# Performance work log

Measured on AMD Instinct MI355X. Metric: run time of the kernel, lower is better.

The kernel has to match this reference:

```python
import jax, jax.numpy as jnp
import numpy as np

VOCAB = 64
EMB = 128
H = 256
OUT = 1
NUM_IN = 7
NUM_OUT = 4
B = 64
S = 2048
D_IN = EMB + NUM_OUT  # input_dim to the 1x1 convs


def setup_inputs() -> dict:
    key = jax.random.key(0)
    ks = jax.random.split(key, 12)
    ev = jax.random.randint(ks[0], (B, S, 1), 0, VOCAB).astype(jnp.float32)
    num = jax.random.normal(ks[1], (B, S, NUM_IN), dtype=jnp.float32)
    X = jnp.concatenate([ev, num], axis=-1)  # [B,S,1+NUM_IN]
    sc = lambda fan_in: 1.0 / np.sqrt(fan_in)
    return {
        "X": X,
        "emb": jax.random.normal(ks[2], (VOCAB, EMB), dtype=jnp.float32),
        "num_W": jax.random.normal(ks[3], (NUM_IN, NUM_OUT), dtype=jnp.float32) * sc(NUM_IN),
        "num_b": jnp.zeros((NUM_OUT,), jnp.float32),
        "Wf": jax.random.normal(ks[4], (D_IN, 3 * H), dtype=jnp.float32) * sc(D_IN),
        "bf": jnp.zeros((3 * H,), jnp.float32),
        "Wb": jax.random.normal(ks[5], (D_IN, 3 * H), dtype=jnp.float32) * sc(D_IN),
        "bb": jnp.zeros((3 * H,), jnp.float32),
        "Mu": jax.random.normal(ks[6], (2 * H, 1), dtype=jnp.float32) * sc(2 * H),
        "out_W": jax.random.normal(ks[7], (2 * H, OUT), dtype=jnp.float32) * sc(2 * H),
        "out_b": jnp.zeros((OUT,), jnp.float32),
    }


def _fo_pool(conv_out):
    # conv_out: [B, S, 3H] (already time-ordered as desired). Returns [B, S, H]
    Z, F, O = jnp.split(conv_out, 3, axis=-1)  # O computed but unused (as in source)
    Z = jnp.tanh(Z)
    F = jax.nn.sigmoid(F)
    # scan over time with state [B, H]
    Zt = jnp.swapaxes(Z, 0, 1)  # [S,B,H]
    Ft = jnp.swapaxes(F, 0, 1)
    h0 = jnp.zeros(Z.shape[::2][:1] + Z.shape[2:], Z.dtype) if False else jnp.zeros((Z.shape[0], Z.shape[2]), Z.dtype)
    def step(h, zf):
        z, f = zf
        h = f * h + (1.0 - f) * z
        return h, h
    _, hs = jax.lax.scan(step, h0, (Zt, Ft))  # [S,B,H] in scan order
    return jnp.swapaxes(hs, 0, 1)  # [B,S,H]


def reference(X, emb, num_W, num_b, Wf, bf, Wb, bb, Mu, out_W, out_b):
    ev = X[:, :, 0].astype(jnp.int32)            # event ids
    num = X[:, :, 1:]                             # numeric features [B,S,7]
    e = emb[ev]                                   # [B,S,EMB]
    n = num @ num_W + num_b                       # [B,S,NUM_OUT]
    x = jnp.concatenate([e, n], axis=-1)          # [B,S,D_IN]
    cf = x @ Wf + bf                              # 1x1 conv == pointwise linear, [B,S,3H]
    cb = x @ Wb + bb
    h_fwd = _fo_pool(cf)                          # [B,S,H], time order
    # backward direction: source iterates t = S-1..0 and stacks in append order
    h_bwd = _fo_pool(cb[:, ::-1, :])              # [B,S,H], reversed-time order (faithful)
    hc = jnp.concatenate([h_fwd, h_bwd], axis=-1) # [B,S,2H]
    scores = hc @ Mu                              # [B,S,1]
    w = jax.nn.softmax(scores, axis=1)
    ctx = jnp.sum(hc * w, axis=1)                 # [B,2H]
    return ctx @ out_W + out_b                    # [B,OUT]
```

## Files before the change

kernel.cpp:

```cpp
#include <hip/hip_runtime.h>
#include <stdint.h>

#define VOCABN 64
#define EMBN   128
#define HDIM   256
#define NUMIN  7
#define BN     64
#define SN     2048
#define TWOH   512
#define SEG    32
#define SEGLEN 64

#define CZ 2.8853900818f
#define CF 1.4426950409f

__device__ __forceinline__ float rcpf(float x){ return __builtin_amdgcn_rcpf(x); }

__device__ __forceinline__ float fast_exp2(float x){
#if __has_builtin(__builtin_amdgcn_exp2f)
    return __builtin_amdgcn_exp2f(x);
#else
    return exp2f(x);
#endif
}

__device__ __forceinline__ float2 pk_fma_blo(float2 a, float2 b, float2 c){
    float2 d;
    asm("v_pk_fma_f32 %0, %1, %2, %3 op_sel_hi:[0,1,1]" : "=v"(d) : "v"(a), "v"(b), "v"(c));
    return d;
}
__device__ __forceinline__ float2 pk_fma_bhi(float2 a, float2 b, float2 c){
    float2 d;
    asm("v_pk_fma_f32 %0, %1, %2, %3 op_sel:[1,0,0] op_sel_hi:[1,1,1]" : "=v"(d) : "v"(a), "v"(b), "v"(c));
    return d;
}

__device__ __forceinline__ uint32_t cvt_pk_bf16(float a, float b){
    uint32_t r;
    asm("v_cvt_pk_bf16_f32 %0, %1, %2" : "=v"(r) : "v"(a), "v"(b));
    return r;
}

__device__ __forceinline__ float waveRedDpp(float x){
    x += __int_as_float(__builtin_amdgcn_update_dpp(0, __float_as_int(x), 0x111, 0xf, 0xf, false));
    x += __int_as_float(__builtin_amdgcn_update_dpp(0, __float_as_int(x), 0x112, 0xf, 0xf, false));
    x += __int_as_float(__builtin_amdgcn_update_dpp(0, __float_as_int(x), 0x114, 0xf, 0xf, false));
    x += __int_as_float(__builtin_amdgcn_update_dpp(0, __float_as_int(x), 0x118, 0xf, 0xf, false));
    x += __int_as_float(__builtin_amdgcn_update_dpp(0, __float_as_int(x), 0x142, 0xa, 0xf, false));
    x += __int_as_float(__builtin_amdgcn_update_dpp(0, __float_as_int(x), 0x143, 0xc, 0xf, false));
    return x;
}

__global__ __launch_bounds__(256) void k0_prep(const float* __restrict__ X, float* __restrict__ Xp)
{
    const int r = blockIdx.x*256 + threadIdx.x;
    const float4* src = (const float4*)(X + (size_t)r*8);
    const float4 a = src[0], b4 = src[1];
    float4* dst = (float4*)(Xp + (size_t)r*8);
    dst[0] = make_float4(a.y, a.z, a.w, b4.x);
    dst[1] = make_float4(b4.y, b4.z, b4.w, __int_as_float((int)a.x * (HDIM*8)));
}

__global__ __launch_bounds__(512) void k1_tables(
    const float* __restrict__ emb, const float* __restrict__ num_W, const float* __restrict__ num_b,
    const float* __restrict__ Wf, const float* __restrict__ bf,
    const float* __restrict__ Wb, const float* __restrict__ bb,
    float* __restrict__ T, float* __restrict__ U)
{
    const int blk = blockIdx.x;
    const int c = threadIdx.x;
    const int jj = c & (HDIM-1);
    const int g = c >> 8;
    const int col = g*HDIM + jj;
    const float gs = g ? CF : CZ;
    const int comp = ((jj >> 7) << 1) + g;
    const int rowj = jj & 127;
    if (blk < 2*VOCABN) {
        const int dir = blk & 1, v = blk >> 1;
        const float* W    = dir ? Wb : Wf;
        const float* bias = dir ? bb : bf;
        float acc = bias[col];
        const float* e = emb + (size_t)v*EMBN;
        #pragma unroll 8
        for (int k=0;k<EMBN;++k) acc = fmaf(e[k], W[(size_t)k*768 + col], acc);
        #pragma unroll
        for (int m=0;m<4;++m)    acc = fmaf(num_b[m], W[(size_t)(EMBN+m)*768 + col], acc);
        T[(((size_t)dir*VOCABN + v)*128 + rowj)*4 + comp] = acc * gs;
    } else {
        const int dir = blk - 2*VOCABN;
        const float* W = dir ? Wb : Wf;
        #pragma unroll
        for (int i=0;i<NUMIN;++i){
            float acc = 0.f;
            #pragma unroll
            for (int m=0;m<4;++m) acc = fmaf(num_W[i*4+m], W[(size_t)(EMBN+m)*768 + col], acc);
            U[(((size_t)dir*8 + i)*128 + rowj)*4 + comp] = acc * gs;
        }
    }
}

template<int MODE>
__global__ __launch_bounds__(128) void k2_scan(
    const float* __restrict__ Xp, const float* __restrict__ T, const float* __restrict__ U,
    const float* __restrict__ Mu, const float* __restrict__ w,
    const float* __restrict__ hstart,
    float* __restrict__ aArr, float* __restrict__ cArr,
    float* __restrict__ swp, float* __restrict__ ctxp, uint32_t* __restrict__ h2)
{
    const int bid = blockIdx.x;
    const int seg = bid & (SEG-1);
    const int dir = (bid >> 5) & 1;
    const int b   = bid >> 6;
    const int j   = threadIdx.x;
    const int blk = (b*2+dir)*SEG + seg;
    const size_t segIdx = (size_t)blk*HDIM + j;

    const char* Tb = (const char*)T + (size_t)dir*VOCABN*2048;
    const float4* Ud4 = (const float4*)U + (size_t)dir*8*128;
    const float4 u0q = Ud4[0*128+j], u1q = Ud4[1*128+j], u2q = Ud4[2*128+j],
                 u3q = Ud4[3*128+j], u4q = Ud4[4*128+j], u5q = Ud4[5*128+j],
                 u6q = Ud4[6*128+j];
    const float2 uLo0 = make_float2(u0q.x,u0q.y), uHi0 = make_float2(u0q.z,u0q.w);
    const float2 uLo1 = make_float2(u1q.x,u1q.y), uHi1 = make_float2(u1q.z,u1q.w);
    const float2 uLo2 = make_float2(u2q.x,u2q.y), uHi2 = make_float2(u2q.z,u2q.w);
    const float2 uLo3 = make_float2(u3q.x,u3q.y), uHi3 = make_float2(u3q.z,u3q.w);
    const float2 uLo4 = make_float2(u4q.x,u4q.y), uHi4 = make_float2(u4q.z,u4q.w);
    const float2 uLo5 = make_float2(u5q.x,u5q.y), uHi5 = make_float2(u5q.z,u5q.w);
    const float2 uLo6 = make_float2(u6q.x,u6q.y), uHi6 = make_float2(u6q.z,u6q.w);
    const float muLo = (MODE==1 || MODE==3) ? Mu[dir*HDIM + j]       : 0.f;
    const float muHi = (MODE==1 || MODE==3) ? Mu[dir*HDIM + j + 128] : 0.f;

    const int sBeg = seg*SEGLEN;
    const float* wb = w + (size_t)b*SN + sBeg;
    const int j16 = j*16;

    __shared__ float4 xlds[SEGLEN][2];
    __shared__ int    evb[SEGLEN];

    {
        const int r = j >> 1, half = j & 1;
        const int gp = b*SN + (dir ? (SN-1-(sBeg+r)) : (sBeg+r));
        const float4 v4 = *(const float4*)(Xp + (size_t)gp*8 + half*4);
        xlds[r][half] = v4;
        if (half) evb[r] = __float_as_int(v4.w);
    }
    __syncthreads();

    float hLo = (MODE==0) ? 0.f : hstart[segIdx];
    float hHi = (MODE==0) ? 0.f : hstart[segIdx + 128];
    float aaccLo = 1.f, aaccHi = 1.f;
    float ctxLo = 0.f, ctxHi = 0.f;
    float hpLo = 0.f, hpHi = 0.f;
    float* swpp = swp + (size_t)(b*4 + dir*2 + (j>>6))*SN + sBeg;
    uint32_t* h2p = h2 + (size_t)blk*(SEGLEN/2)*HDIM + j;

    float4 xa0 = xlds[0][0], xb0 = xlds[0][1];
    float4 xa1 = xlds[1][0], xb1 = xlds[1][1];
    int e3 = evb[3];
    float4 t0 = *(const float4*)(Tb + (uint32_t)(evb[0] + j16));
    float4 t1 = *(const float4*)(Tb + (uint32_t)(evb[1] + j16));
    float4 t2 = *(const float4*)(Tb + (uint32_t)(evb[2] + j16));

    #pragma unroll 8
    for (int si=0; si<SEGLEN; ++si){
        const float4 t3 = *(const float4*)(Tb + (uint32_t)(e3 + j16));
        const int i2 = (si+2 < SEGLEN) ? si+2 : SEGLEN-1;
        const float4 xan = xlds[i2][0];
        const float4 xbn = xlds[i2][1];
        const int i4 = (si+4 < SEGLEN) ? si+4 : SEGLEN-1;
        const int en = evb[i4];

        const float2 xp01 = make_float2(xa0.x, xa0.y);
        const float2 xp23 = make_float2(xa0.z, xa0.w);
        const float2 xp45 = make_float2(xb0.x, xb0.y);
        const float2 xp6e = make_float2(xb0.z, xb0.w);
        float2 zfLo = make_float2(t0.x, t0.y);
        float2 zfHi = make_float2(t0.z, t0.w);
        zfLo = pk_fma_blo(xp01, uLo0, zfLo);  zfHi = pk_fma_blo(xp01, uHi0, zfHi);
        zfLo = pk_fma_bhi(xp01, uLo1, zfLo);  zfHi = pk_fma_bhi(xp01, uHi1, zfHi);
        zfLo = pk_fma_blo(xp23, uLo2, zfLo);  zfHi = pk_fma_blo(xp23, uHi2, zfHi);
        zfLo = pk_fma_bhi(xp23, uLo3, zfLo);  zfHi = pk_fma_bhi(xp23, uHi3, zfHi);
        zfLo = pk_fma_blo(xp45, uLo4, zfLo);  zfHi = pk_fma_blo(xp45, uHi4, zfHi);
        zfLo = pk_fma_bhi(xp45, uLo5, zfLo);  zfHi = pk_fma_bhi(xp45, uHi5, zfHi);
        zfLo = pk_fma_blo(xp6e, uLo6, zfLo);  zfHi = pk_fma_blo(xp6e, uHi6, zfHi);

        const float e2zL = fast_exp2(zfLo.x), efL = fast_exp2(zfLo.y);
        const float e2zH = fast_exp2(zfHi.x), efH = fast_exp2(zfHi.y);
        const float a2L = 1.f + e2zL, a1L = 1.f + efL;
        const float a2H = 1.f + e2zH, a1H = 1.f + efH;
        const float rL = rcpf(a1L * a2L);
        const float rH = rcpf(a1H * a2H);
        hLo = fmaf(efL * hLo, a2L, e2zL - 1.f) * rL;
        hHi = fmaf(efH * hHi, a2H, e2zH - 1.f) * rH;

        if (MODE==0){
            aaccLo *= efL * a2L * rL;
            aaccHi *= efH * a2H * rH;
        } else if (MODE==1 || MODE==3){
            float pr = waveRedDpp(fmaf(hHi, muHi, hLo * muLo));
            if ((j & 63) == 63) swpp[si] = pr;
            if (MODE==1){
                if (si & 1){
                    h2p[0]   = cvt_pk_bf16(hpLo, hLo);
                    h2p[128] = cvt_pk_bf16(hpHi, hHi);
                    h2p += HDIM;
                } else { hpLo = hLo; hpHi = hHi; }
            }
        } else {
            const float ws_ = wb[si];
            ctxLo = fmaf(ws_, hLo, ctxLo);
            ctxHi = fmaf(ws_, hHi, ctxHi);
        }
        xa0=xa1; xb0=xb1; xa1=xan; xb1=xbn;
        t0=t1; t1=t2; t2=t3; e3=en;
    }
    if (MODE==0){
        aArr[segIdx] = aaccLo; aArr[segIdx+128] = aaccHi;
        cArr[segIdx] = hLo;    cArr[segIdx+128] = hHi;
    }
    if (MODE==2){ ctxp[segIdx] = ctxLo; ctxp[segIdx+128] = ctxHi; }
}

__global__ __launch_bounds__(256) void k_compose(const float* __restrict__ aArr, const float* __restrict__ cArr,
                                                 float* __restrict__ hstart)
{
    const int bd = blockIdx.x;
    const int j  = threadIdx.x;
    float h = 0.f;
    #pragma unroll
    for (int seg=0; seg<SEG; ++seg){
        const size_t idx = ((size_t)bd*SEG + seg)*HDIM + j;
        hstart[idx] = h;
        h = fmaf(aArr[idx], h, cArr[idx]);
    }
}

__global__ __launch_bounds__(256) void k3_softmax(const float* __restrict__ swp, float* __restrict__ w)
{
    __shared__ float sc[SN];
    __shared__ float red[4];
    const int b = blockIdx.x, t = threadIdx.x;
    for (int s=t; s<SN; s+=256){
        float acc = 0.f;
        #pragma unroll
        for (int r=0;r<4;++r) acc += swp[((size_t)b*4 + r)*SN + s];
        sc[s] = acc;
    }
    __syncthreads();
    float m = -3.4e38f;
    for (int s=t; s<SN; s+=256) m = fmaxf(m, sc[s]);
    #pragma unroll
    for (int o=32;o;o>>=1) m = fmaxf(m, __shfl_xor(m,o,64));
    if ((t&63)==0) red[t>>6] = m;
    __syncthreads();
    m = fmaxf(fmaxf(red[0],red[1]), fmaxf(red[2],red[3]));
    float zs = 0.f;
    for (int s=t; s<SN; s+=256){
        float e = __expf(sc[s]-m);
        sc[s] = e;
        zs += e;
    }
    #pragma unroll
    for (int o=32;o;o>>=1) zs += __shfl_xor(zs,o,64);
    __syncthreads();
    if ((t&63)==0) red[t>>6] = zs;
    __syncthreads();
    zs = red[0]+red[1]+red[2]+red[3];
    float invz = rcpf(zs);
    for (int s=t; s<SN; s+=256) w[(size_t)b*SN + s] = sc[s]*invz;
}

__global__ __launch_bounds__(256) void k4_ctx(const uint32_t* __restrict__ h2, const float* __restrict__ w,
                                              float* __restrict__ ctxp)
{
    const int bid = blockIdx.x;
    const int seg = bid & (SEG-1);
    const int dir = (bid >> 5) & 1;
    const int b   = bid >> 6;
    const int blk = (b*2+dir)*SEG + seg;
    const int j   = threadIdx.x;
    const float* wb = w + (size_t)b*SN + seg*SEGLEN;
    const uint32_t* hp = h2 + (size_t)blk*(SEGLEN/2)*HDIM + j;
    float acc = 0.f;
    #pragma unroll 8
    for (int si2=0; si2<SEGLEN/2; ++si2){
        const uint32_t pk = hp[(size_t)si2*HDIM];
        const float hlo = __int_as_float(pk << 16);
        const float hhi = __int_as_float(pk & 0xffff0000u);
        acc = fmaf(wb[2*si2  ], hlo, acc);
        acc = fmaf(wb[2*si2+1], hhi, acc);
    }
    ctxp[(size_t)blk*HDIM + j] = acc;
}

__global__ __launch_bounds__(512) void k5_out(const float* __restrict__ ctxp, const float* __restrict__ out_W,
                                              const float* __restrict__ out_b, float* __restrict__ out)
{
    __shared__ float red[8];
    const int b = blockIdx.x, c = threadIdx.x;
    const int dir = c >> 8, j = c & (HDIM-1);
    float acc = 0.f;
    #pragma unroll
    for (int seg=0; seg<SEG; ++seg)
        acc += ctxp[((size_t)(b*2+dir)*SEG + seg)*HDIM + j];
    float p = acc * out_W[c];
    #pragma unroll
    for (int o=32;o;o>>=1) p += __shfl_xor(p,o,64);
    if ((c&63)==0) red[c>>6] = p;
    __syncthreads();
    if (c==0){
        float t = 0.f;
        #pragma unroll
        for (int r=0;r<8;++r) t += red[r];
        out[b] = t + out_b[0];
    }
}

extern "C" void kernel_launch(void* const* d_in, const int* in_sizes, int n_in,
                              void* d_out, int out_size, void* d_ws, size_t ws_size,
                              hipStream_t stream)
{
    const float* X     = (const float*)d_in[0];
    const float* emb   = (const float*)d_in[1];
    const float* num_W = (const float*)d_in[2];
    const float* num_b = (const float*)d_in[3];
    const float* Wf    = (const float*)d_in[4];
    const float* bf    = (const float*)d_in[5];
    const float* Wb    = (const float*)d_in[6];
    const float* bb    = (const float*)d_in[7];
    const float* Mu    = (const float*)d_in[8];
    const float* out_W = (const float*)d_in[9];
    const float* out_b = (const float*)d_in[10];
    float* out = (float*)d_out;

    float* ws = (float*)d_ws;
    size_t off = 0;
    float* swp   = ws + off; off += (size_t)BN*4*SN;
    float* w     = ws + off; off += (size_t)BN*SN;
    float* T     = ws + off; off += (size_t)2*VOCABN*TWOH;
    float* U     = ws + off; off += (size_t)2*8*TWOH;
    float* aArr  = ws + off; off += (size_t)BN*2*SEG*HDIM;
    float* cArr  = ws + off; off += (size_t)BN*2*SEG*HDIM;
    float* hstart= ws + off; off += (size_t)BN*2*SEG*HDIM;
    float* ctxp  = ws + off; off += (size_t)BN*2*SEG*HDIM;
    float* Xp    = ws + off; off += (size_t)BN*SN*8;
    uint32_t* h2 = (uint32_t*)(ws + off);
    off += (size_t)BN*2*SEG*(SEGLEN/2)*HDIM;
    const bool useStore = ((size_t)off * sizeof(float)) <= ws_size;

    hipLaunchKernelGGL(k0_prep,     dim3(BN*SN/256),   dim3(256), 0, stream, X, Xp);
    hipLaunchKernelGGL(k1_tables,   dim3(2*VOCABN+2),  dim3(512), 0, stream,
                       emb, num_W, num_b, Wf, bf, Wb, bb, T, U);
    hipLaunchKernelGGL(k2_scan<0>,  dim3(BN*2*SEG),    dim3(128), 0, stream,
                       Xp, T, U, Mu, w, hstart, aArr, cArr, swp, ctxp, h2);
    hipLaunchKernelGGL(k_compose,   dim3(BN*2),        dim3(256), 0, stream,
                       aArr, cArr, hstart);
    if (useStore) {
        hipLaunchKernelGGL(k2_scan<1>, dim3(BN*2*SEG), dim3(128), 0, stream,
                           Xp, T, U, Mu, w, hstart, aArr, cArr, swp, ctxp, h2);
        hipLaunchKernelGGL(k3_softmax, dim3(BN),       dim3(256), 0, stream, swp, w);
        hipLaunchKernelGGL(k4_ctx,     dim3(BN*2*SEG), dim3(256), 0, stream, h2, w, ctxp);
    } else {
        hipLaunchKernelGGL(k2_scan<3>, dim3(BN*2*SEG), dim3(128), 0, stream,
                           Xp, T, U, Mu, w, hstart, aArr, cArr, swp, ctxp, h2);
        hipLaunchKernelGGL(k3_softmax, dim3(BN),       dim3(256), 0, stream, swp, w);
        hipLaunchKernelGGL(k2_scan<2>, dim3(BN*2*SEG), dim3(128), 0, stream,
                           Xp, T, U, Mu, w, hstart, aArr, cArr, swp, ctxp, h2);
    }
    hipLaunchKernelGGL(k5_out,      dim3(BN),          dim3(512), 0, stream,
                       ctxp, out_W, out_b, out);
}
```

Baseline: 151.3 us.

## Shrink scan blocks to one wavefront handling four hidden channel pairs per thread

The scan kernel now runs 64 threads per block instead of 128, and each thread carries four hidden-state channel pairs instead of two. This removes the cross-wave partial score reduction: one wavefront reduces the attention score and the softmax sums two partials instead of four. The bf16 hidden-state store is re-laid so each word packs two channels of one timestep, and k4_ctx is changed to match. The cost is more registers and more serial work per thread, with fewer threads overall to hide the latency of the table gathers.

```diff
diff --git a/kernel.cpp b/kernel.cpp
--- a/kernel.cpp
+++ b/kernel.cpp
@@ -100,7 +100,7 @@
 }
 
 template<int MODE>
-__global__ __launch_bounds__(128) void k2_scan(
+__global__ __launch_bounds__(64) void k2_scan(
     const float* __restrict__ Xp, const float* __restrict__ T, const float* __restrict__ U,
     const float* __restrict__ Mu, const float* __restrict__ w,
     const float* __restrict__ hstart,
@@ -117,108 +117,145 @@
 
     const char* Tb = (const char*)T + (size_t)dir*VOCABN*2048;
     const float4* Ud4 = (const float4*)U + (size_t)dir*8*128;
-    const float4 u0q = Ud4[0*128+j], u1q = Ud4[1*128+j], u2q = Ud4[2*128+j],
-                 u3q = Ud4[3*128+j], u4q = Ud4[4*128+j], u5q = Ud4[5*128+j],
-                 u6q = Ud4[6*128+j];
-    const float2 uLo0 = make_float2(u0q.x,u0q.y), uHi0 = make_float2(u0q.z,u0q.w);
-    const float2 uLo1 = make_float2(u1q.x,u1q.y), uHi1 = make_float2(u1q.z,u1q.w);
-    const float2 uLo2 = make_float2(u2q.x,u2q.y), uHi2 = make_float2(u2q.z,u2q.w);
-    const float2 uLo3 = make_float2(u3q.x,u3q.y), uHi3 = make_float2(u3q.z,u3q.w);
-    const float2 uLo4 = make_float2(u4q.x,u4q.y), uHi4 = make_float2(u4q.z,u4q.w);
-    const float2 uLo5 = make_float2(u5q.x,u5q.y), uHi5 = make_float2(u5q.z,u5q.w);
-    const float2 uLo6 = make_float2(u6q.x,u6q.y), uHi6 = make_float2(u6q.z,u6q.w);
-    const float muLo = (MODE==1 || MODE==3) ? Mu[dir*HDIM + j]       : 0.f;
-    const float muHi = (MODE==1 || MODE==3) ? Mu[dir*HDIM + j + 128] : 0.f;
+    float2 uA0[NUMIN], uA1[NUMIN], uB0[NUMIN], uB1[NUMIN];
+    #pragma unroll
+    for (int i=0;i<NUMIN;++i){
+        const float4 qa = Ud4[i*128 + j];
+        const float4 qb = Ud4[i*128 + j + 64];
+        uA0[i] = make_float2(qa.x, qa.y);  uA1[i] = make_float2(qa.z, qa.w);
+        uB0[i] = make_float2(qb.x, qb.y);  uB1[i] = make_float2(qb.z, qb.w);
+    }
+    float muA0=0.f, muB0=0.f, muA1=0.f, muB1=0.f;
+    if (MODE==1 || MODE==3){
+        muA0 = Mu[dir*HDIM + j];       muB0 = Mu[dir*HDIM + j + 64];
+        muA1 = Mu[dir*HDIM + j + 128]; muB1 = Mu[dir*HDIM + j + 192];
+    }
 
     const int sBeg = seg*SEGLEN;
     const float* wb = w + (size_t)b*SN + sBeg;
     const int j16 = j*16;
 
-    __shared__ float4 xlds[SEGLEN][2];
-    __shared__ int    evb[SEGLEN];
+    __shared__ float4 xlds[SEGLEN+4][2];
+    __shared__ int    evb[SEGLEN+4];
 
     {
-        const int r = j >> 1, half = j & 1;
-        const int gp = b*SN + (dir ? (SN-1-(sBeg+r)) : (sBeg+r));
-        const float4 v4 = *(const float4*)(Xp + (size_t)gp*8 + half*4);
-        xlds[r][half] = v4;
-        if (half) evb[r] = __float_as_int(v4.w);
-    }
-    __syncthreads();
-
-    float hLo = (MODE==0) ? 0.f : hstart[segIdx];
-    float hHi = (MODE==0) ? 0.f : hstart[segIdx + 128];
-    float aaccLo = 1.f, aaccHi = 1.f;
-    float ctxLo = 0.f, ctxHi = 0.f;
-    float hpLo = 0.f, hpHi = 0.f;
-    float* swpp = swp + (size_t)(b*4 + dir*2 + (j>>6))*SN + sBeg;
-    uint32_t* h2p = h2 + (size_t)blk*(SEGLEN/2)*HDIM + j;
+        auto stage = [&](int c){
+            const int r = c >> 1, half = c & 1;
+            const int rr = (r < SEGLEN) ? r : SEGLEN-1;
+            const int spos = sBeg + rr;
+            const int gp = b*SN + (dir ? (SN-1-spos) : spos);
+            const float4 v4 = *(const float4*)(Xp + (size_t)gp*8 + half*4);
+            xlds[r][half] = v4;
+            if (half) evb[r] = __float_as_int(v4.w);
+        };
+        stage(j); stage(j + 64);
+        if (j < 8) stage(128 + j);
+    }
+    __syncthreads();
+
+    float hA0, hA1, hB0, hB1;
+    if (MODE==0){ hA0=hA1=hB0=hB1=0.f; }
+    else {
+        hA0 = hstart[segIdx];       hB0 = hstart[segIdx + 64];
+        hA1 = hstart[segIdx + 128]; hB1 = hstart[segIdx + 192];
+    }
+    float aA0=1.f, aA1=1.f, aB0=1.f, aB1=1.f;
+    float cA0=0.f, cA1=0.f, cB0=0.f, cB1=0.f;
+    float* swpp = swp + (size_t)(b*2 + dir)*SN + sBeg;
+    uint32_t* h2p = h2 + (size_t)blk*SEGLEN*128 + j;
 
     float4 xa0 = xlds[0][0], xb0 = xlds[0][1];
     float4 xa1 = xlds[1][0], xb1 = xlds[1][1];
-    int e3 = evb[3];
-    float4 t0 = *(const float4*)(Tb + (uint32_t)(evb[0] + j16));
-    float4 t1 = *(const float4*)(Tb + (uint32_t)(evb[1] + j16));
-    float4 t2 = *(const float4*)(Tb + (uint32_t)(evb[2] + j16));
-
-    #pragma unroll 8
+    int e2 = evb[2];
+    const char* tq0 = Tb + (uint32_t)evb[0];
+    const char* tq1 = Tb + (uint32_t)evb[1];
+    float4 tA0 = *(const float4*)(tq0 + j16), tB0 = *(const float4*)(tq0 + j16 + 1024);
+    float4 tA1 = *(const float4*)(tq1 + j16), tB1 = *(const float4*)(tq1 + j16 + 1024);
+
+    #pragma unroll 4
     for (int si=0; si<SEGLEN; ++si){
-        const float4 t3 = *(const float4*)(Tb + (uint32_t)(e3 + j16));
-        const int i2 = (si+2 < SEGLEN) ? si+2 : SEGLEN-1;
-        const float4 xan = xlds[i2][0];
-        const float4 xbn = xlds[i2][1];
-        const int i4 = (si+4 < SEGLEN) ? si+4 : SEGLEN-1;
-        const int en = evb[i4];
+        const char* tq2 = Tb + (uint32_t)e2;
+        const float4 tA2 = *(const float4*)(tq2 + j16);
+        const float4 tB2 = *(const float4*)(tq2 + j16 + 1024);
+        const float4 xan = xlds[si+2][0];
+        const float4 xbn = xlds[si+2][1];
+        const int en = evb[si+3];
 
         const float2 xp01 = make_float2(xa0.x, xa0.y);
         const float2 xp23 = make_float2(xa0.z, xa0.w);
         const float2 xp45 = make_float2(xb0.x, xb0.y);
         const float2 xp6e = make_float2(xb0.z, xb0.w);
-        float2 zfLo = make_float2(t0.x, t0.y);
-        float2 zfHi = make_float2(t0.z, t0.w);
-        zfLo = pk_fma_blo(xp01, uLo0, zfLo);  zfHi = pk_fma_blo(xp01, uHi0, zfHi);
-        zfLo = pk_fma_bhi(xp01, uLo1, zfLo);  zfHi = pk_fma_bhi(xp01, uHi1, zfHi);
-        zfLo = pk_fma_blo(xp23, uLo2, zfLo);  zfHi = pk_fma_blo(xp23, uHi2, zfHi);
-        zfLo = pk_fma_bhi(xp23, uLo3, zfLo);  zfHi = pk_fma_bhi(xp23, uHi3, zfHi);
-        zfLo = pk_fma_blo(xp45, uLo4, zfLo);  zfHi = pk_fma_blo(xp45, uHi4, zfHi);
-        zfLo = pk_fma_bhi(xp45, uLo5, zfLo);  zfHi = pk_fma_bhi(xp45, uHi5, zfHi);
-        zfLo = pk_fma_blo(xp6e, uLo6, zfLo);  zfHi = pk_fma_blo(xp6e, uHi6, zfHi);
-
-        const float e2zL = fast_exp2(zfLo.x), efL = fast_exp2(zfLo.y);
-        const float e2zH = fast_exp2(zfHi.x), efH = fast_exp2(zfHi.y);
-        const float a2L = 1.f + e2zL, a1L = 1.f + efL;
-        const float a2H = 1.f + e2zH, a1H = 1.f + efH;
-        const float rL = rcpf(a1L * a2L);
-        const float rH = rcpf(a1H * a2H);
-        hLo = fmaf(efL * hLo, a2L, e2zL - 1.f) * rL;
-        hHi = fmaf(efH * hHi, a2H, e2zH - 1.f) * rH;
-
-        if (MODE==0){
-            aaccLo *= efL * a2L * rL;
-            aaccHi *= efH * a2H * rH;
-        } else if (MODE==1 || MODE==3){
-            float pr = waveRedDpp(fmaf(hHi, muHi, hLo * muLo));
-            if ((j & 63) == 63) swpp[si] = pr;
+        float2 zA0 = make_float2(tA0.x, tA0.y);
+        float2 zA1 = make_float2(tA0.z, tA0.w);
+        float2 zB0 = make_float2(tB0.x, tB0.y);
+        float2 zB1 = make_float2(tB0.z, tB0.w);
+        zA0 = pk_fma_blo(xp01, uA0[0], zA0); zA1 = pk_fma_blo(xp01, uA1[0], zA1);
+        zB0 = pk_fma_blo(xp01, uB0[0], zB0); zB1 = pk_fma_blo(xp01, uB1[0], zB1);
+        zA0 = pk_fma_bhi(xp01, uA0[1], zA0); zA1 = pk_fma_bhi(xp01, uA1[1], zA1);
+        zB0 = pk_fma_bhi(xp01, uB0[1], zB0); zB1 = pk_fma_bhi(xp01, uB1[1], zB1);
+        zA0 = pk_fma_blo(xp23, uA0[2], zA0); zA1 = pk_fma_blo(xp23, uA1[2], zA1);
+        zB0 = pk_fma_blo(xp23, uB0[2], zB0); zB1 = pk_fma_blo(xp23, uB1[2], zB1);
+        zA0 = pk_fma_bhi(xp23, uA0[3], zA0); zA1 = pk_fma_bhi(xp23, uA1[3], zA1);
+        zB0 = pk_fma_bhi(xp23, uB0[3], zB0); zB1 = pk_fma_bhi(xp23, uB1[3], zB1);
+        zA0 = pk_fma_blo(xp45, uA0[4], zA0); zA1 = pk_fma_blo(xp45, uA1[4], zA1);
+        zB0 = pk_fma_blo(xp45, uB0[4], zB0); zB1 = pk_fma_blo(xp45, uB1[4], zB1);
+        zA0 = pk_fma_bhi(xp45, uA0[5], zA0); zA1 = pk_fma_bhi(xp45, uA1[5], zA1);
+        zB0 = pk_fma_bhi(xp45, uB0[5], zB0); zB1 = pk_fma_bhi(xp45, uB1[5], zB1);
+        zA0 = pk_fma_blo(xp6e, uA0[6], zA0); zA1 = pk_fma_blo(xp6e, uA1[6], zA1);
+        zB0 = pk_fma_blo(xp6e, uB0[6], zB0); zB1 = pk_fma_blo(xp6e, uB1[6], zB1);
+
+        {
+            const float e2z = fast_exp2(zA0.x), ef = fast_exp2(zA0.y);
+            const float a2 = 1.f + e2z, a1 = 1.f + ef;
+            const float r_ = rcpf(a1 * a2);
+            hA0 = fmaf(ef * hA0, a2, e2z - 1.f) * r_;
+            if (MODE==0) aA0 *= ef * a2 * r_;
+        }
+        {
+            const float e2z = fast_exp2(zA1.x), ef = fast_exp2(zA1.y);
+            const float a2 = 1.f + e2z, a1 = 1.f + ef;
+            const float r_ = rcpf(a1 * a2);
+            hA1 = fmaf(ef * hA1, a2, e2z - 1.f) * r_;
+            if (MODE==0) aA1 *= ef * a2 * r_;
+        }
+        {
+            const float e2z = fast_exp2(zB0.x), ef = fast_exp2(zB0.y);
+            const float a2 = 1.f + e2z, a1 = 1.f + ef;
+            const float r_ = rcpf(a1 * a2);
+            hB0 = fmaf(ef * hB0, a2, e2z - 1.f) * r_;
+            if (MODE==0) aB0 *= ef * a2 * r_;
+        }
+        {
+            const float e2z = fast_exp2(zB1.x), ef = fast_exp2(zB1.y);
+            const float a2 = 1.f + e2z, a1 = 1.f + ef;
+            const float r_ = rcpf(a1 * a2);
+            hB1 = fmaf(ef * hB1, a2, e2z - 1.f) * r_;
+            if (MODE==0) aB1 *= ef * a2 * r_;
+        }
+
+        if (MODE==1 || MODE==3){
+            float pr = fmaf(hB1, muB1, fmaf(hA1, muA1, fmaf(hB0, muB0, hA0 * muA0)));
+            pr = waveRedDpp(pr);
+            if (j == 63) swpp[si] = pr;
             if (MODE==1){
-                if (si & 1){
-                    h2p[0]   = cvt_pk_bf16(hpLo, hLo);
-                    h2p[128] = cvt_pk_bf16(hpHi, hHi);
-                    h2p += HDIM;
-                } else { hpLo = hLo; hpHi = hHi; }
+                h2p[si*128]      = cvt_pk_bf16(hA0, hA1);
+                h2p[si*128 + 64] = cvt_pk_bf16(hB0, hB1);
             }
-        } else {
+        } else if (MODE==2){
             const float ws_ = wb[si];
-            ctxLo = fmaf(ws_, hLo, ctxLo);
-            ctxHi = fmaf(ws_, hHi, ctxHi);
+            cA0 = fmaf(ws_, hA0, cA0); cA1 = fmaf(ws_, hA1, cA1);
+            cB0 = fmaf(ws_, hB0, cB0); cB1 = fmaf(ws_, hB1, cB1);
         }
         xa0=xa1; xb0=xb1; xa1=xan; xb1=xbn;
-        t0=t1; t1=t2; t2=t3; e3=en;
+        tA0=tA1; tB0=tB1; tA1=tA2; tB1=tB2; e2=en;
     }
     if (MODE==0){
-        aArr[segIdx] = aaccLo; aArr[segIdx+128] = aaccHi;
-        cArr[segIdx] = hLo;    cArr[segIdx+128] = hHi;
-    }
-    if (MODE==2){ ctxp[segIdx] = ctxLo; ctxp[segIdx+128] = ctxHi; }
+        aArr[segIdx] = aA0;  aArr[segIdx+64] = aB0;  aArr[segIdx+128] = aA1;  aArr[segIdx+192] = aB1;
+        cArr[segIdx] = hA0;  cArr[segIdx+64] = hB0;  cArr[segIdx+128] = hA1;  cArr[segIdx+192] = hB1;
+    }
+    if (MODE==2){
+        ctxp[segIdx] = cA0;  ctxp[segIdx+64] = cB0;  ctxp[segIdx+128] = cA1;  ctxp[segIdx+192] = cB1;
+    }
 }
 
 __global__ __launch_bounds__(256) void k_compose(const float* __restrict__ aArr, const float* __restrict__ cArr,
@@ -243,7 +280,7 @@
     for (int s=t; s<SN; s+=256){
         float acc = 0.f;
         #pragma unroll
-        for (int r=0;r<4;++r) acc += swp[((size_t)b*4 + r)*SN + s];
+        for (int r=0;r<2;++r) acc += swp[((size_t)b*2 + r)*SN + s];
         sc[s] = acc;
     }
     __syncthreads();
@@ -270,7 +307,7 @@
     for (int s=t; s<SN; s+=256) w[(size_t)b*SN + s] = sc[s]*invz;
 }
 
-__global__ __launch_bounds__(256) void k4_ctx(const uint32_t* __restrict__ h2, const float* __restrict__ w,
+__global__ __launch_bounds__(128) void k4_ctx(const uint32_t* __restrict__ h2, const float* __restrict__ w,
                                               float* __restrict__ ctxp)
 {
     const int bid = blockIdx.x;
@@ -278,19 +315,21 @@
     const int dir = (bid >> 5) & 1;
     const int b   = bid >> 6;
     const int blk = (b*2+dir)*SEG + seg;
-    const int j   = threadIdx.x;
+    const int p   = threadIdx.x;
     const float* wb = w + (size_t)b*SN + seg*SEGLEN;
-    const uint32_t* hp = h2 + (size_t)blk*(SEGLEN/2)*HDIM + j;
-    float acc = 0.f;
+    const uint32_t* hp = h2 + (size_t)blk*SEGLEN*128 + p;
+    float acc0 = 0.f, acc1 = 0.f;
     #pragma unroll 8
-    for (int si2=0; si2<SEGLEN/2; ++si2){
-        const uint32_t pk = hp[(size_t)si2*HDIM];
-        const float hlo = __int_as_float(pk << 16);
-        const float hhi = __int_as_float(pk & 0xffff0000u);
-        acc = fmaf(wb[2*si2  ], hlo, acc);
-        acc = fmaf(wb[2*si2+1], hhi, acc);
-    }
-    ctxp[(size_t)blk*HDIM + j] = acc;
+    for (int si=0; si<SEGLEN; ++si){
+        const uint32_t pk = hp[si*128];
+        const float hv0 = __int_as_float(pk << 16);
+        const float hv1 = __int_as_float(pk & 0xffff0000u);
+        const float ws_ = wb[si];
+        acc0 = fmaf(ws_, hv0, acc0);
+        acc1 = fmaf(ws_, hv1, acc1);
+    }
+    ctxp[(size_t)blk*HDIM + p]       = acc0;
+    ctxp[(size_t)blk*HDIM + p + 128] = acc1;
 }
 
 __global__ __launch_bounds__(512) void k5_out(const float* __restrict__ ctxp, const float* __restrict__ out_W,
@@ -335,7 +374,7 @@
 
     float* ws = (float*)d_ws;
     size_t off = 0;
-    float* swp   = ws + off; off += (size_t)BN*4*SN;
+    float* swp   = ws + off; off += (size_t)BN*2*SN;
     float* w     = ws + off; off += (size_t)BN*SN;
     float* T     = ws + off; off += (size_t)2*VOCABN*TWOH;
     float* U     = ws + off; off += (size_t)2*8*TWOH;
@@ -345,26 +384,26 @@
     float* ctxp  = ws + off; off += (size_t)BN*2*SEG*HDIM;
     float* Xp    = ws + off; off += (size_t)BN*SN*8;
     uint32_t* h2 = (uint32_t*)(ws + off);
-    off += (size_t)BN*2*SEG*(SEGLEN/2)*HDIM;
+    off += (size_t)BN*2*SEG*SEGLEN*128;
     const bool useStore = ((size_t)off * sizeof(float)) <= ws_size;
 
     hipLaunchKernelGGL(k0_prep,     dim3(BN*SN/256),   dim3(256), 0, stream, X, Xp);
     hipLaunchKernelGGL(k1_tables,   dim3(2*VOCABN+2),  dim3(512), 0, stream,
                        emb, num_W, num_b, Wf, bf, Wb, bb, T, U);
-    hipLaunchKernelGGL(k2_scan<0>,  dim3(BN*2*SEG),    dim3(128), 0, stream,
+    hipLaunchKernelGGL(k2_scan<0>,  dim3(BN*2*SEG),    dim3(64), 0, stream,
                        Xp, T, U, Mu, w, hstart, aArr, cArr, swp, ctxp, h2);
     hipLaunchKernelGGL(k_compose,   dim3(BN*2),        dim3(256), 0, stream,
                        aArr, cArr, hstart);
     if (useStore) {
-        hipLaunchKernelGGL(k2_scan<1>, dim3(BN*2*SEG), dim3(128), 0, stream,
+        hipLaunchKernelGGL(k2_scan<1>, dim3(BN*2*SEG), dim3(64), 0, stream,
                            Xp, T, U, Mu, w, hstart, aArr, cArr, swp, ctxp, h2);
         hipLaunchKernelGGL(k3_softmax, dim3(BN),       dim3(256), 0, stream, swp, w);
-        hipLaunchKernelGGL(k4_ctx,     dim3(BN*2*SEG), dim3(256), 0, stream, h2, w, ctxp);
+        hipLaunchKernelGGL(k4_ctx,     dim3(BN*2*SEG), dim3(128), 0, stream, h2, w, ctxp);
     } else {
-        hipLaunchKernelGGL(k2_scan<3>, dim3(BN*2*SEG), dim3(128), 0, stream,
+        hipLaunchKernelGGL(k2_scan<3>, dim3(BN*2*SEG), dim3(64), 0, stream,
                            Xp, T, U, Mu, w, hstart, aArr, cArr, swp, ctxp, h2);
         hipLaunchKernelGGL(k3_softmax, dim3(BN),       dim3(256), 0, stream, swp, w);
-        hipLaunchKernelGGL(k2_scan<2>, dim3(BN*2*SEG), dim3(128), 0, stream,
+        hipLaunchKernelGGL(k2_scan<2>, dim3(BN*2*SEG), dim3(64), 0, stream,
                            Xp, T, U, Mu, w, hstart, aArr, cArr, swp, ctxp, h2);
     }
     hipLaunchKernelGGL(k5_out,      dim3(BN),          dim3(512), 0, stream,
```

Result: faster. 148.0 us (median of 2 runs) (-2.1%).
